# Optimization experiments

Measured on AMD Instinct MI355X. Metric: run time of the kernel, lower is better.

## Reference

```python
import jax, jax.numpy as jnp
import numpy as np
from jax import lax

NAG = 3          # hardcoded in the torch module (query slices, catted_torches)
B = 4096         # batch_size per agent
H = 128          # hidden_dim
HEADS = 8
AD = H // HEADS  # attend_dim
STATE, ACT, SCAN = 48, 2, 256
OUTF, HID = 10, 256
NFEAT = 32 * (SCAN - 6)  # conv output features (two VALID convs: k5 then k3)
EPS = 1e-5

def leaky(x):
    return jnp.where(x >= 0, x, 0.01 * x)

def setup_inputs() -> dict:
    key = jax.random.key(0)
    ks = iter(jax.random.split(key, 40))
    def rn(shape, scale=0.05):
        return jax.random.normal(next(ks), shape, dtype=jnp.float32) * scale
    return {
        'obs':  jax.random.normal(next(ks), (NAG * B, STATE), jnp.float32),
        'acts': jax.random.normal(next(ks), (NAG * B, ACT), jnp.float32),
        'scan': jax.random.normal(next(ks), (NAG * B, SCAN), jnp.float32),
        'conv_w1': rn((32, 1, 5)),  'conv_b1': jnp.zeros((32,), jnp.float32),
        'conv_w2': rn((32, 32, 3)), 'conv_b2': jnp.zeros((32,), jnp.float32),
        'fc_w1': rn((256, NFEAT), 0.01), 'fc_b1': jnp.zeros((256,), jnp.float32),
        'fc_w2': rn((OUTF, 256)),        'fc_b2': jnp.zeros((OUTF,), jnp.float32),
        'enc_w': rn((H, STATE + ACT + OUTF)), 'enc_b': jnp.zeros((H,), jnp.float32),
        'Wk': rn((HEADS, AD, H)),
        'Wv': rn((HEADS, AD, H)), 'bv': jnp.zeros((HEADS, AD), jnp.float32),
        'Wq': rn((NAG, HEADS, AD, H)),
        'q1_w1': rn((HID, 2 * H)), 'q1_b1': jnp.zeros((HID,), jnp.float32),
        'q1_w2': rn((HID, HID)),   'q1_b2': jnp.zeros((HID,), jnp.float32),
        'q1_w3': rn((1, HID)),     'q1_b3': jnp.zeros((1,), jnp.float32),
        'q2_w1': rn((HID, 2 * H)), 'q2_b1': jnp.zeros((HID,), jnp.float32),
        'q2_w2': rn((HID, HID)),   'q2_b2': jnp.zeros((HID,), jnp.float32),
        'q2_w3': rn((1, HID)),     'q2_b3': jnp.zeros((1,), jnp.float32),
    }

def reference(obs, acts, scan, conv_w1, conv_b1, conv_w2, conv_b2,
              fc_w1, fc_b1, fc_w2, fc_b2, enc_w, enc_b, Wk, Wv, bv, Wq,
              q1_w1, q1_b1, q1_w2, q1_b2, q1_w3, q1_b3,
              q2_w1, q2_b1, q2_w2, q2_b2, q2_w3, q2_b3):
    dn = ('NCH', 'OIH', 'NCH')
    x = scan[:, None, :]                                            # [N,1,L]
    x = lax.conv_general_dilated(x, conv_w1, (1,), 'VALID', dimension_numbers=dn)
    x = jax.nn.relu(x + conv_b1[None, :, None])
    x = lax.conv_general_dilated(x, conv_w2, (1,), 'VALID', dimension_numbers=dn)
    x = jax.nn.relu(x + conv_b2[None, :, None])
    x = x.reshape(x.shape[0], -1)                                   # [N, NFEAT]
    x = jax.nn.relu(x @ fc_w1.T + fc_b1)
    feats = x @ fc_w2.T + fc_b2                                     # [N, OUTF]

    inps = jnp.concatenate([obs, acts, feats], axis=1)
    mu, var = inps.mean(0), inps.var(0)                             # BatchNorm1d (train, no affine)
    normed = (inps - mu) / jnp.sqrt(var + EPS)
    sa = leaky(normed @ enc_w.T + enc_b).reshape(NAG, B, H)         # [ag,B,H]

    keys = jnp.einsum('gbh,ndh->ngbd', sa, Wk)                      # [hd,ag,B,ad]
    vals = leaky(jnp.einsum('gbh,ndh->ngbd', sa, Wv) + bv[:, None, None, :])
    q = jnp.einsum('gbh,gndh->gnbd', sa, Wq)                        # [ag,hd,B,ad]

    logits = jnp.einsum('gnbd,nobd->gnbo', q, keys) / np.sqrt(AD)   # [ag,hd,B,ag]
    self_mask = jnp.eye(NAG, dtype=bool)[:, None, None, :]          # exclude own agent
    logits = jnp.where(self_mask, -jnp.inf, logits)
    w = jax.nn.softmax(logits, axis=-1)
    other = jnp.einsum('gnbo,nobd->gnbd', w, vals)                  # [ag,hd,B,ad]
    other = other.transpose(0, 2, 1, 3).reshape(NAG, B, H)          # heads concatenated

    emb = jnp.concatenate([sa, other], axis=2).reshape(NAG * B, 2 * H)

    def mlp(x, w1, b1, w2, b2, w3, b3):
        x = jax.nn.relu(x @ w1.T + b1)
        x = jax.nn.relu(x @ w2.T + b2)
        return x @ w3.T + b3

    q1 = mlp(emb, q1_w1, q1_b1, q1_w2, q1_b2, q1_w3, q1_b3)
    q2 = mlp(emb, q2_w1, q2_b1, q2_w2, q2_b2, q2_w3, q2_b3)
    return (q1, q2)
```

## Files before the change

kernel.cpp:

```cpp
#include <hip/hip_runtime.h>
#include <hip/hip_bf16.h>
#include <cstdint>
#include <cstddef>

typedef unsigned short u16;
typedef __attribute__((ext_vector_type(8))) __bf16 bf16x8;
typedef __attribute__((ext_vector_type(4))) float f32x4;

__device__ __forceinline__ u16 f2b(float f) {
  __hip_bfloat16 h = __float2bfloat16(f);
  return *reinterpret_cast<u16*>(&h);
}
__device__ __forceinline__ uint32_t pk2(float a, float b) {
  __hip_bfloat162 h = __float22bfloat162_rn(make_float2(a, b));
  return *reinterpret_cast<uint32_t*>(&h);
}
__device__ __forceinline__ float b2f(u16 u) {
  union { float f; uint32_t i; } x; x.i = ((uint32_t)u) << 16; return x.f;
}
__device__ __forceinline__ f32x4 mfma16(bf16x8 a, bf16x8 b, f32x4 c) {
  return __builtin_amdgcn_mfma_f32_16x16x32_bf16(a, b, c, 0, 0, 0);
}
__device__ __forceinline__ void async16(const void* g, void* l) {
  __builtin_amdgcn_global_load_lds((const __attribute__((address_space(1))) uint32_t*)g,
                                   (__attribute__((address_space(3))) uint32_t*)l, 16, 0, 0);
}

__global__ __launch_bounds__(256) void w1_perm(const float* __restrict__ w,
                                               u16* __restrict__ o) {
  __shared__ float L[8000];
  int j = blockIdx.x, tid = threadIdx.x;
  for (int i = tid; i < 8000; i += 256) L[i] = w[(size_t)j * 8000 + i];
  __syncthreads();
  for (int i = tid; i < 8000; i += 256) {
    int tt = i >> 5, c2 = i & 31;
    o[(size_t)j * 8000 + i] = f2b(L[c2 * 250 + tt]);
  }
}

struct CvtArgs {
  const float* src[8];
  u16* dst[8];
  int cum[9];
};
__global__ __launch_bounds__(256) void f2b_multi(CvtArgs a, float* stats) {
  int i = blockIdx.x * 256 + threadIdx.x;
  if (blockIdx.x == 0 && threadIdx.x < 128) stats[threadIdx.x] = 0.f;
  int seg = 0;
  #pragma unroll
  for (int s = 1; s < 8; ++s) if (i >= a.cum[s]) seg = s;
  if (i < a.cum[8]) {
    int off = i - a.cum[seg];
    if (seg == 7) {
      int c2 = off / 96, rem = off - c2 * 96, kk = rem >> 5, c1 = rem & 31;
      a.dst[7][off] = f2b(a.src[7][(c2 * 32 + c1) * 3 + kk]);
    } else {
      a.dst[seg][off] = f2b(a.src[seg][off]);
    }
  }
}

__global__ __launch_bounds__(256) void conv_fused(
    const float* __restrict__ scan, const float* __restrict__ cw1,
    const float* __restrict__ cb1, const u16* __restrict__ w2g,
    const float* __restrict__ cb2, u16* __restrict__ x, int row0) {
  __shared__ float s[260];
  __shared__ __align__(16) u16 h1T[258 * 40];
  int tid = threadIdx.x;
  int lrow = blockIdx.x;
  int lane = tid & 63, wv = tid >> 6;
  int l15 = lane & 15, quad = lane >> 4;
  s[tid] = scan[(size_t)(row0 + lrow) * 256 + tid];
  if (tid < 4) s[256 + tid] = 0.f;
  if (tid < 240) h1T[252 * 40 + tid] = 0;
  bf16x8 wfrag[2][3];
  #pragma unroll
  for (int i = 0; i < 2; ++i)
    #pragma unroll
    for (int kk = 0; kk < 3; ++kk)
      wfrag[i][kk] = *(const bf16x8*)&w2g[(i * 16 + l15) * 96 + kk * 32 + quad * 8];
  float bias[2][4];
  #pragma unroll
  for (int i = 0; i < 2; ++i)
    #pragma unroll
    for (int r = 0; r < 4; ++r) bias[i][r] = cb2[i * 16 + quad * 4 + r];
  __syncthreads();
  {
    int cpair = tid & 15, pr = tid >> 4;
    int c0 = cpair * 2;
    float wA[5], wB[5];
    #pragma unroll
    for (int k = 0; k < 5; ++k) { wA[k] = cw1[c0 * 5 + k]; wB[k] = cw1[c0 * 5 + 5 + k]; }
    float bA = cb1[c0], bB = cb1[c0 + 1];
    float sv[20];
    int p0 = pr * 16;
    #pragma unroll
    for (int j = 0; j < 5; ++j) {
      f32x4 v = *(const f32x4*)&s[p0 + 4 * j];
      sv[4 * j] = v[0]; sv[4 * j + 1] = v[1]; sv[4 * j + 2] = v[2]; sv[4 * j + 3] = v[3];
    }
    #pragma unroll
    for (int ii = 0; ii < 16; ++ii) {
      float va = bA, vb = bB;
      #pragma unroll
      for (int k = 0; k < 5; ++k) {
        va += sv[ii + k] * wA[k];
        vb += sv[ii + k] * wB[k];
      }
      int p = p0 + ii;
      if (p < 252) {
        *(uint32_t*)&h1T[p * 40 + c0] = pk2(fmaxf(va, 0.f), fmaxf(vb, 0.f));
      }
    }
  }
  __syncthreads();
  f32x4 zero = {0.f, 0.f, 0.f, 0.f};
  f32x4 acc[4][2];
  #pragma unroll
  for (int jj = 0; jj < 4; ++jj) { acc[jj][0] = zero; acc[jj][1] = zero; }
  #pragma unroll
  for (int kk = 0; kk < 3; ++kk) {
    #pragma unroll
    for (int jj = 0; jj < 4; ++jj) {
      int t = (wv * 4 + jj) * 16 + l15 + kk;
      bf16x8 h = *(const bf16x8*)&h1T[t * 40 + quad * 8];
      acc[jj][0] = mfma16(wfrag[0][kk], h, acc[jj][0]);
      acc[jj][1] = mfma16(wfrag[1][kk], h, acc[jj][1]);
    }
  }
  __syncthreads();
  #pragma unroll
  for (int jj = 0; jj < 4; ++jj) {
    int t = (wv * 4 + jj) * 16 + l15;
    if (t < 250) {
      #pragma unroll
      for (int i = 0; i < 2; ++i) {
        float v0 = fmaxf(acc[jj][i][0] + bias[i][0], 0.f);
        float v1 = fmaxf(acc[jj][i][1] + bias[i][1], 0.f);
        float v2 = fmaxf(acc[jj][i][2] + bias[i][2], 0.f);
        float v3 = fmaxf(acc[jj][i][3] + bias[i][3], 0.f);
        uint2 pr2; pr2.x = pk2(v0, v1); pr2.y = pk2(v2, v3);
        *(uint2*)&h1T[t * 40 + i * 16 + quad * 4] = pr2;
      }
    }
  }
  __syncthreads();
  u16* xr = x + (size_t)lrow * 8000;
  #pragma unroll
  for (int it = 0; it < 4; ++it) {
    int e0 = (it * 256 + tid) * 8;
    if (e0 < 8000) {
      int t = e0 >> 5, c8 = (e0 >> 3) & 3;
      bf16x8 v = *(const bf16x8*)&h1T[t * 40 + c8 * 8];
      *(bf16x8*)&xr[e0] = v;
    }
  }
}

template <int MODE>
__global__ __launch_bounds__(256) void gemm_bt(
    const u16* __restrict__ A, int lda, const u16* __restrict__ W,
    const float* __restrict__ bias, float* __restrict__ outF,
    u16* __restrict__ outB, int ldo, int nst, int wq_sel, size_t out_zoff) {
  __shared__ __align__(16) u16 As[2][128 * 64];
  __shared__ __align__(16) u16 Bs[2][128 * 64];
  int tid = threadIdx.x;
  int m0 = blockIdx.y * 128, n0 = blockIdx.x * 128;
  if (wq_sel) W += (size_t)(blockIdx.y >> 5) * wq_sel;
  int kbase = blockIdx.z * nst * 64;
  if (MODE == 0) outF += (size_t)blockIdx.z * out_zoff;
  const u16* Ap = A + (size_t)m0 * lda + kbase;
  const u16* Wp = W + (size_t)n0 * lda + kbase;
  int lane = tid & 63, wv = tid >> 6;
  int l15 = lane & 15, quad = lane >> 4;
  int wm = (wv >> 1) * 64, wn = (wv & 1) * 64;
  f32x4 zero = {0.f, 0.f, 0.f, 0.f};
  f32x4 acc[4][4];
  #pragma unroll
  for (int i = 0; i < 4; ++i)
    #pragma unroll
    for (int j = 0; j < 4; ++j) acc[i][j] = zero;

  int srow[4], soff[4], sdst[4];
  #pragma unroll
  for (int it = 0; it < 4; ++it) {
    int c = it * 256 + tid;
    int row = c >> 3, slot = c & 7;
    srow[it] = row;
    soff[it] = ((slot ^ (row & 7)) * 8);
    sdst[it] = c * 8;
  }
  int rslot[2];
  rslot[0] = ((quad ^ (l15 & 7)) * 8);
  rslot[1] = (((4 + quad) ^ (l15 & 7)) * 8);

  #pragma unroll 1
  for (int st = 0; st < nst; ++st) {
    if (st == 0) {
      #pragma unroll
      for (int it = 0; it < 4; ++it) {
        async16(Ap + (size_t)srow[it] * lda + soff[it], &As[0][sdst[it]]);
        async16(Wp + (size_t)srow[it] * lda + soff[it], &Bs[0][sdst[it]]);
      }
    }
    __syncthreads();
    if (st + 1 < nst) {
      const u16* An = Ap + (st + 1) * 64;
      const u16* Wn = Wp + (st + 1) * 64;
      u16* Ad = &As[(st + 1) & 1][0];
      u16* Bd = &Bs[(st + 1) & 1][0];
      #pragma unroll
      for (int it = 0; it < 4; ++it) {
        async16(An + (size_t)srow[it] * lda + soff[it], Ad + sdst[it]);
        async16(Wn + (size_t)srow[it] * lda + soff[it], Bd + sdst[it]);
      }
    }
    const u16* Ab = &As[st & 1][0];
    const u16* Bb = &Bs[st & 1][0];
    #pragma unroll
    for (int s = 0; s < 2; ++s) {
      bf16x8 af[4], bfr[4];
      #pragma unroll
      for (int i = 0; i < 4; ++i)
        af[i] = *(const bf16x8*)&Ab[(wm + i * 16 + l15) * 64 + rslot[s]];
      #pragma unroll
      for (int j = 0; j < 4; ++j)
        bfr[j] = *(const bf16x8*)&Bb[(wn + j * 16 + l15) * 64 + rslot[s]];
      #pragma unroll
      for (int i = 0; i < 4; ++i)
        #pragma unroll
        for (int j = 0; j < 4; ++j) acc[i][j] = mfma16(af[i], bfr[j], acc[i][j]);
    }
  }
  #pragma unroll
  for (int i = 0; i < 4; ++i) {
    int mb = m0 + wm + i * 16 + quad * 4;
    #pragma unroll
    for (int j = 0; j < 4; ++j) {
      int n = n0 + wn + j * 16 + l15;
      float bv_ = (MODE == 1 || MODE == 2) ? bias[n] : 0.f;
      #pragma unroll
      for (int r = 0; r < 4; ++r) {
        float v = acc[i][j][r];
        if (MODE == 0) {
          outF[(size_t)(mb + r) * ldo + n] = v;
        } else {
          v += bv_;
          if (MODE == 1) v = fmaxf(v, 0.f);
          if (MODE == 2) v = v >= 0.f ? v : 0.01f * v;
          outB[(size_t)(mb + r) * ldo + n] = f2b(v);
        }
      }
    }
  }
}

__global__ __launch_bounds__(256) void fc2_stats(
    const float* __restrict__ hparts, const float* __restrict__ b1,
    const float* __restrict__ w2, const float* __restrict__ b2,
    const float* __restrict__ obs, const float* __restrict__ acts,
    float* __restrict__ inps, float* __restrict__ stats) {
  __shared__ float hL[32 * 260];
  __shared__ float w2L[10 * 260];
  __shared__ float b1L[256];
  __shared__ float ipL[32 * 61];
  int tid = threadIdx.x, r0 = blockIdx.x * 32;
  b1L[tid] = b1[tid];
  for (int i = tid; i < 2560; i += 256) w2L[(i >> 8) * 260 + (i & 255)] = w2[i];
  for (int i = tid; i < 32 * 48; i += 256) {
    int r = i / 48, f = i - r * 48;
    ipL[r * 61 + f] = obs[(size_t)(r0 + r) * 48 + f];
  }
  if (tid < 64) {
    int r = tid >> 1, f = tid & 1;
    ipL[r * 61 + 48 + f] = acts[(size_t)(r0 + r) * 2 + f];
  }
  __syncthreads();
  const size_t HS = (size_t)12288 * 256;
  for (int i = tid; i < 32 * 256; i += 256) {
    int r = i >> 8, c = i & 255;
    size_t g = (size_t)(r0 + r) * 256 + c;
    float v = b1L[c] + hparts[g] + hparts[g + HS] + hparts[g + 2 * HS] +
              hparts[g + 3 * HS] + hparts[g + 4 * HS];
    hL[r * 260 + c] = fmaxf(v, 0.f);
  }
  __syncthreads();
  {
    int r = tid >> 3, ob = tid & 7;
    for (int o = ob; o < 10; o += 8) {
      float a = 0.f;
      #pragma unroll 8
      for (int c = 0; c < 256; ++c) a += hL[r * 260 + c] * w2L[o * 260 + c];
      ipL[r * 61 + 50 + o] = a + b2[o];
    }
  }
  __syncthreads();
  for (int i = tid; i < 32 * 60; i += 256) {
    int r = i / 60, f = i - r * 60;
    inps[(size_t)(r0 + r) * 64 + f] = ipL[r * 61 + f];
  }
  if (tid < 60) {
    float s = 0.f, s2 = 0.f;
    for (int r = 0; r < 32; ++r) {
      float v = ipL[r * 61 + tid];
      s += v; s2 += v * v;
    }
    atomicAdd(&stats[tid], s);
    atomicAdd(&stats[64 + tid], s2);
  }
}

__global__ __launch_bounds__(256) void enc_kernel(
    const float* __restrict__ inps, const float* __restrict__ stats,
    const float* __restrict__ enc_w, const float* __restrict__ enc_b,
    u16* __restrict__ sab) {
  __shared__ float ewL[128 * 61];
  __shared__ float nrm[32 * 61];
  __shared__ float ebL[128];
  __shared__ float muL[60], ivL[60];
  int tid = threadIdx.x, r0 = blockIdx.x * 32;
  if (tid < 128) ebL[tid] = enc_b[tid];
  if (tid < 60) {
    float s = stats[tid], s2 = stats[64 + tid];
    float mu = s * (1.f / 12288.f);
    float var = s2 * (1.f / 12288.f) - mu * mu;
    muL[tid] = mu;
    ivL[tid] = rsqrtf(var + 1e-5f);
  }
  for (int i = tid; i < 128 * 60; i += 256) {
    int h = i / 60, f = i - h * 60;
    ewL[h * 61 + f] = enc_w[i];
  }
  __syncthreads();
  for (int i = tid; i < 32 * 60; i += 256) {
    int r = i / 60, f = i - r * 60;
    nrm[r * 61 + f] = (inps[(size_t)(r0 + r) * 64 + f] - muL[f]) * ivL[f];
  }
  __syncthreads();
  for (int i = tid; i < 32 * 128; i += 256) {
    int r = i >> 7, h = i & 127;
    float a = ebL[h];
    #pragma unroll 4
    for (int f = 0; f < 60; ++f) a += nrm[r * 61 + f] * ewL[h * 61 + f];
    a = a >= 0.f ? a : 0.01f * a;
    sab[(size_t)(r0 + r) * 128 + h] = f2b(a);
  }
}

__global__ __launch_bounds__(128) void attn_combine(
    const u16* __restrict__ qb, const u16* __restrict__ keysb,
    const u16* __restrict__ valsb, const u16* __restrict__ sab,
    u16* __restrict__ emb) {
  __shared__ float qL[3][128], kL[3][128], vL[3][128];
  __shared__ float lg[3][8][3], wgt[3][8][3];
  int b = blockIdx.x, t = threadIdx.x;
  #pragma unroll
  for (int o = 0; o < 3; ++o) {
    size_t base = (size_t)(o * 4096 + b) * 128 + t;
    qL[o][t] = b2f(qb[base]);
    kL[o][t] = b2f(keysb[base]);
    vL[o][t] = b2f(valsb[base]);
  }
  __syncthreads();
  if (t < 72) {
    int g = t / 24, n = (t / 3) % 8, o = t % 3;
    float a = 0.f;
    #pragma unroll
    for (int d = 0; d < 16; ++d) a += qL[g][n * 16 + d] * kL[o][n * 16 + d];
    lg[g][n][o] = (o == g) ? -1e30f : a * 0.25f;
  }
  __syncthreads();
  if (t < 24) {
    int g = t / 8, n = t % 8;
    float m = fmaxf(fmaxf(lg[g][n][0], lg[g][n][1]), lg[g][n][2]);
    float e0 = expf(lg[g][n][0] - m), e1 = expf(lg[g][n][1] - m),
          e2 = expf(lg[g][n][2] - m);
    float inv = 1.f / (e0 + e1 + e2);
    wgt[g][n][0] = e0 * inv; wgt[g][n][1] = e1 * inv; wgt[g][n][2] = e2 * inv;
  }
  __syncthreads();
  int n = t >> 4, d = t & 15;
  #pragma unroll
  for (int g = 0; g < 3; ++g) {
    float o_ = wgt[g][n][0] * vL[0][n * 16 + d] +
               wgt[g][n][1] * vL[1][n * 16 + d] +
               wgt[g][n][2] * vL[2][n * 16 + d];
    size_t rbase = (size_t)(g * 4096 + b) * 256;
    emb[rbase + 128 + t] = f2b(o_);
    emb[rbase + t] = sab[(size_t)(g * 4096 + b) * 128 + t];
  }
}

__global__ __launch_bounds__(256) void final_dot(
    const u16* __restrict__ t2a, const u16* __restrict__ t2b,
    const float* __restrict__ w3a, const float* __restrict__ b3a,
    const float* __restrict__ w3b, const float* __restrict__ b3b,
    float* __restrict__ out) {
  int wv = threadIdx.x >> 6, lane = threadIdx.x & 63;
  int row = blockIdx.x * 4 + wv;
  float sa_ = 0.f, sb_ = 0.f;
  #pragma unroll
  for (int e = 0; e < 4; ++e) {
    int c = lane * 4 + e;
    sa_ += b2f(t2a[(size_t)row * 256 + c]) * w3a[c];
    sb_ += b2f(t2b[(size_t)row * 256 + c]) * w3b[c];
  }
  #pragma unroll
  for (int off = 32; off; off >>= 1) {
    sa_ += __shfl_down(sa_, off);
    sb_ += __shfl_down(sb_, off);
  }
  if (lane == 0) {
    out[row] = sa_ + b3a[0];
    out[12288 + row] = sb_ + b3b[0];
  }
}

extern "C" void kernel_launch(void* const* d_in, const int* in_sizes, int n_in,
                              void* d_out, int out_size, void* d_ws,
                              size_t ws_size, hipStream_t stream) {
  const float* obs  = (const float*)d_in[0];
  const float* acts = (const float*)d_in[1];
  const float* scan = (const float*)d_in[2];
  const float* cw1  = (const float*)d_in[3];
  const float* cb1  = (const float*)d_in[4];
  const float* cw2  = (const float*)d_in[5];
  const float* cb2  = (const float*)d_in[6];
  const float* fw1  = (const float*)d_in[7];
  const float* fb1  = (const float*)d_in[8];
  const float* fw2  = (const float*)d_in[9];
  const float* fb2  = (const float*)d_in[10];
  const float* encw = (const float*)d_in[11];
  const float* encb = (const float*)d_in[12];
  const float* Wk   = (const float*)d_in[13];
  const float* Wv   = (const float*)d_in[14];
  const float* bv   = (const float*)d_in[15];
  const float* Wq   = (const float*)d_in[16];
  const float* q1w1 = (const float*)d_in[17];
  const float* q1b1 = (const float*)d_in[18];
  const float* q1w2 = (const float*)d_in[19];
  const float* q1b2 = (const float*)d_in[20];
  const float* q1w3 = (const float*)d_in[21];
  const float* q1b3 = (const float*)d_in[22];
  const float* q2w1 = (const float*)d_in[23];
  const float* q2b1 = (const float*)d_in[24];
  const float* q2w2 = (const float*)d_in[25];
  const float* q2b2 = (const float*)d_in[26];
  const float* q2w3 = (const float*)d_in[27];
  const float* q2b3 = (const float*)d_in[28];
  float* out = (float*)d_out;
  char* ws = (char*)d_ws;
  if (ws_size < 166009856u) return;

  u16*   x     = (u16*)(ws + 0);
  u16*   w1b   = (u16*)(ws + 98304000);
  float* hpart = (float*)(ws + 102400000);
  float* stats = (float*)(ws + 165314560);
  u16*   wkb   = (u16*)(ws + 165315584);
  u16*   wvb   = (u16*)(ws + 165348352);
  u16*   wqb   = (u16*)(ws + 165381120);
  u16*   m1a   = (u16*)(ws + 165479424);
  u16*   m2a   = (u16*)(ws + 165610496);
  u16*   m1b   = (u16*)(ws + 165741568);
  u16*   m2b   = (u16*)(ws + 165872640);
  u16*   w2g   = (u16*)(ws + 166003712);
  float* inps  = (float*)(ws + 0);
  u16*   sab   = (u16*)(ws + 3145728);
  u16*   keysb = (u16*)(ws + 6291456);
  u16*   valsb = (u16*)(ws + 9437184);
  u16*   qb    = (u16*)(ws + 12582912);
  u16*   embb  = (u16*)(ws + 15728640);
  u16*   t1a   = (u16*)(ws + 22020096);
  u16*   t2a   = (u16*)(ws + 28311552);
  u16*   t1b   = (u16*)(ws + 34603008);
  u16*   t2b   = (u16*)(ws + 40894464);

  w1_perm<<<256, 256, 0, stream>>>(fw1, w1b);
  CvtArgs ca;
  ca.src[0] = Wk;  ca.src[1] = Wv;  ca.src[2] = Wq;  ca.src[3] = q1w1;
  ca.src[4] = q1w2; ca.src[5] = q2w1; ca.src[6] = q2w2; ca.src[7] = cw2;
  ca.dst[0] = wkb; ca.dst[1] = wvb; ca.dst[2] = wqb; ca.dst[3] = m1a;
  ca.dst[4] = m2a; ca.dst[5] = m1b; ca.dst[6] = m2b; ca.dst[7] = w2g;
  const int sz[8] = {16384, 16384, 49152, 65536, 65536, 65536, 65536, 3072};
  int cum = 0;
  ca.cum[0] = 0;
  for (int i = 0; i < 8; ++i) { cum += sz[i]; ca.cum[i + 1] = cum; }
  f2b_multi<<<(cum + 255) / 256, 256, 0, stream>>>(ca, stats);

  for (int s = 0; s < 2; ++s) {
    conv_fused<<<6144, 256, 0, stream>>>(scan, cw1, cb1, w2g, cb2, x, s * 6144);
    gemm_bt<0><<<dim3(2, 48, 5), 256, 0, stream>>>(
        x, 8000, w1b, nullptr, hpart + (size_t)s * 6144 * 256, nullptr, 256,
        25, 0, (size_t)12288 * 256);
  }
  fc2_stats<<<384, 256, 0, stream>>>(hpart, fb1, fw2, fb2, obs, acts, inps, stats);
  enc_kernel<<<384, 256, 0, stream>>>(inps, stats, encw, encb, sab);
  gemm_bt<3><<<dim3(1, 96, 1), 256, 0, stream>>>(sab, 128, wkb, nullptr, nullptr,
                                                 keysb, 128, 2, 0, 0);
  gemm_bt<2><<<dim3(1, 96, 1), 256, 0, stream>>>(sab, 128, wvb, bv, nullptr,
                                                 valsb, 128, 2, 0, 0);
  gemm_bt<3><<<dim3(1, 96, 1), 256, 0, stream>>>(sab, 128, wqb, nullptr, nullptr,
                                                 qb, 128, 2, 16384, 0);
  attn_combine<<<4096, 128, 0, stream>>>(qb, keysb, valsb, sab, embb);
  gemm_bt<1><<<dim3(2, 96, 1), 256, 0, stream>>>(embb, 256, m1a, q1b1, nullptr,
                                                 t1a, 256, 4, 0, 0);
  gemm_bt<1><<<dim3(2, 96, 1), 256, 0, stream>>>(t1a, 256, m2a, q1b2, nullptr,
                                                 t2a, 256, 4, 0, 0);
  gemm_bt<1><<<dim3(2, 96, 1), 256, 0, stream>>>(embb, 256, m1b, q2b1, nullptr,
                                                 t1b, 256, 4, 0, 0);
  gemm_bt<1><<<dim3(2, 96, 1), 256, 0, stream>>>(t1b, 256, m2b, q2b2, nullptr,
                                                 t2b, 256, 4, 0, 0);
  final_dot<<<3072, 256, 0, stream>>>(t2a, t2b, q1w3, q1b3, q2w3, q2b3, out);
}
```

Before: 379.9 us.

## Run conv1 on MFMA, write conv output directly, and batch twin Q-MLP GEMMs

The first convolution (k=5, single input channel) moves from scalar FMAs to a bf16 MFMA, using a zero-padded im2col tile in LDS and a pre-converted padded weight matrix. The second conv's epilogue writes bf16 results straight to global memory, removing an LDS staging pass and a barrier. The two Q-network MLPs are merged into two wider GEMM launches over concatenated weights, using a per-block A-offset for the second layer, which cuts the number of launches. The price is extra LDS for the im2col tile, rounding conv1 inputs to bf16, and uncoalesced 8-byte global stores in the conv epilogue.

```diff
diff --git a/kernel.cpp b/kernel.cpp
--- a/kernel.cpp
+++ b/kernel.cpp
@@ -39,138 +39,152 @@
 }
 
 struct CvtArgs {
-  const float* src[8];
-  u16* dst[8];
-  int cum[9];
+  const float* src[13];
+  void* dst[13];
+  int cum[14];
+  int kind[13];
 };
 __global__ __launch_bounds__(256) void f2b_multi(CvtArgs a, float* stats) {
   int i = blockIdx.x * 256 + threadIdx.x;
   if (blockIdx.x == 0 && threadIdx.x < 128) stats[threadIdx.x] = 0.f;
   int seg = 0;
   #pragma unroll
-  for (int s = 1; s < 8; ++s) if (i >= a.cum[s]) seg = s;
-  if (i < a.cum[8]) {
+  for (int s = 1; s < 13; ++s) if (i >= a.cum[s]) seg = s;
+  if (i < a.cum[13]) {
     int off = i - a.cum[seg];
-    if (seg == 7) {
+    int kind = a.kind[seg];
+    const float* src = a.src[seg];
+    if (kind == 0) {
+      ((u16*)a.dst[seg])[off] = f2b(src[off]);
+    } else if (kind == 1) {
       int c2 = off / 96, rem = off - c2 * 96, kk = rem >> 5, c1 = rem & 31;
-      a.dst[7][off] = f2b(a.src[7][(c2 * 32 + c1) * 3 + kk]);
+      ((u16*)a.dst[seg])[off] = f2b(src[(c2 * 32 + c1) * 3 + kk]);
+    } else if (kind == 2) {
+      int c1 = off >> 5, k = off & 31;
+      ((u16*)a.dst[seg])[off] = f2b(k < 5 ? src[c1 * 5 + k] : 0.f);
     } else {
-      a.dst[seg][off] = f2b(a.src[seg][off]);
+      ((float*)a.dst[seg])[off] = src[off];
     }
   }
 }
 
 __global__ __launch_bounds__(256) void conv_fused(
-    const float* __restrict__ scan, const float* __restrict__ cw1,
+    const float* __restrict__ scan, const u16* __restrict__ w1g,
     const float* __restrict__ cb1, const u16* __restrict__ w2g,
     const float* __restrict__ cb2, u16* __restrict__ x, int row0) {
   __shared__ float s[260];
+  __shared__ __align__(16) u16 A1[256 * 40];
   __shared__ __align__(16) u16 h1T[258 * 40];
   int tid = threadIdx.x;
-  int lrow = blockIdx.x;
   int lane = tid & 63, wv = tid >> 6;
   int l15 = lane & 15, quad = lane >> 4;
-  s[tid] = scan[(size_t)(row0 + lrow) * 256 + tid];
+  s[tid] = scan[(size_t)(row0 + blockIdx.x) * 256 + tid];
   if (tid < 4) s[256 + tid] = 0.f;
-  if (tid < 240) h1T[252 * 40 + tid] = 0;
-  bf16x8 wfrag[2][3];
+  if (tid < 80) h1T[256 * 40 + tid] = 0;
+  bf16x8 w1f[2];
+  w1f[0] = *(const bf16x8*)&w1g[l15 * 32 + quad * 8];
+  w1f[1] = *(const bf16x8*)&w1g[(16 + l15) * 32 + quad * 8];
+  bf16x8 w2f[2][3];
   #pragma unroll
   for (int i = 0; i < 2; ++i)
     #pragma unroll
     for (int kk = 0; kk < 3; ++kk)
-      wfrag[i][kk] = *(const bf16x8*)&w2g[(i * 16 + l15) * 96 + kk * 32 + quad * 8];
-  float bias[2][4];
+      w2f[i][kk] = *(const bf16x8*)&w2g[(i * 16 + l15) * 96 + kk * 32 + quad * 8];
+  float cb1v[2][4], cb2v[2][4];
   #pragma unroll
   for (int i = 0; i < 2; ++i)
     #pragma unroll
-    for (int r = 0; r < 4; ++r) bias[i][r] = cb2[i * 16 + quad * 4 + r];
+    for (int r = 0; r < 4; ++r) {
+      cb1v[i][r] = cb1[i * 16 + quad * 4 + r];
+      cb2v[i][r] = cb2[i * 16 + quad * 4 + r];
+    }
   __syncthreads();
   {
-    int cpair = tid & 15, pr = tid >> 4;
-    int c0 = cpair * 2;
-    float wA[5], wB[5];
-    #pragma unroll
-    for (int k = 0; k < 5; ++k) { wA[k] = cw1[c0 * 5 + k]; wB[k] = cw1[c0 * 5 + 5 + k]; }
-    float bA = cb1[c0], bB = cb1[c0 + 1];
-    float sv[20];
-    int p0 = pr * 16;
-    #pragma unroll
-    for (int j = 0; j < 5; ++j) {
-      f32x4 v = *(const f32x4*)&s[p0 + 4 * j];
-      sv[4 * j] = v[0]; sv[4 * j + 1] = v[1]; sv[4 * j + 2] = v[2]; sv[4 * j + 3] = v[3];
-    }
-    #pragma unroll
-    for (int ii = 0; ii < 16; ++ii) {
-      float va = bA, vb = bB;
-      #pragma unroll
-      for (int k = 0; k < 5; ++k) {
-        va += sv[ii + k] * wA[k];
-        vb += sv[ii + k] * wB[k];
+    union { bf16x8 v; u16 u[8]; } pk;
+    #pragma unroll
+    for (int k = 0; k < 5; ++k) pk.u[k] = f2b(s[tid + k]);
+    pk.u[5] = 0; pk.u[6] = 0; pk.u[7] = 0;
+    *(bf16x8*)&A1[tid * 40] = pk.v;
+    uint4 z = make_uint4(0, 0, 0, 0);
+    *(uint4*)&A1[tid * 40 + 8] = z;
+    *(uint4*)&A1[tid * 40 + 16] = z;
+    *(uint4*)&A1[tid * 40 + 24] = z;
+  }
+  __syncthreads();
+  f32x4 zero = {0.f, 0.f, 0.f, 0.f};
+  {
+    f32x4 acc1[4][2];
+    #pragma unroll
+    for (int nt = 0; nt < 4; ++nt) { acc1[nt][0] = zero; acc1[nt][1] = zero; }
+    #pragma unroll
+    for (int nt = 0; nt < 4; ++nt) {
+      int p = (wv * 4 + nt) * 16 + l15;
+      bf16x8 bfr = *(const bf16x8*)&A1[p * 40 + quad * 8];
+      acc1[nt][0] = mfma16(w1f[0], bfr, acc1[nt][0]);
+      acc1[nt][1] = mfma16(w1f[1], bfr, acc1[nt][1]);
+    }
+    #pragma unroll
+    for (int nt = 0; nt < 4; ++nt) {
+      int p = (wv * 4 + nt) * 16 + l15;
+      #pragma unroll
+      for (int mt = 0; mt < 2; ++mt) {
+        float v0 = fmaxf(acc1[nt][mt][0] + cb1v[mt][0], 0.f);
+        float v1 = fmaxf(acc1[nt][mt][1] + cb1v[mt][1], 0.f);
+        float v2 = fmaxf(acc1[nt][mt][2] + cb1v[mt][2], 0.f);
+        float v3 = fmaxf(acc1[nt][mt][3] + cb1v[mt][3], 0.f);
+        uint2 u; u.x = pk2(v0, v1); u.y = pk2(v2, v3);
+        *(uint2*)&h1T[p * 40 + mt * 16 + quad * 4] = u;
       }
-      int p = p0 + ii;
-      if (p < 252) {
-        *(uint32_t*)&h1T[p * 40 + c0] = pk2(fmaxf(va, 0.f), fmaxf(vb, 0.f));
-      }
-    }
-  }
-  __syncthreads();
-  f32x4 zero = {0.f, 0.f, 0.f, 0.f};
-  f32x4 acc[4][2];
-  #pragma unroll
-  for (int jj = 0; jj < 4; ++jj) { acc[jj][0] = zero; acc[jj][1] = zero; }
+    }
+  }
+  __syncthreads();
+  f32x4 acc2[4][2];
+  #pragma unroll
+  for (int jj = 0; jj < 4; ++jj) { acc2[jj][0] = zero; acc2[jj][1] = zero; }
   #pragma unroll
   for (int kk = 0; kk < 3; ++kk) {
     #pragma unroll
     for (int jj = 0; jj < 4; ++jj) {
       int t = (wv * 4 + jj) * 16 + l15 + kk;
       bf16x8 h = *(const bf16x8*)&h1T[t * 40 + quad * 8];
-      acc[jj][0] = mfma16(wfrag[0][kk], h, acc[jj][0]);
-      acc[jj][1] = mfma16(wfrag[1][kk], h, acc[jj][1]);
-    }
-  }
-  __syncthreads();
+      acc2[jj][0] = mfma16(w2f[0][kk], h, acc2[jj][0]);
+      acc2[jj][1] = mfma16(w2f[1][kk], h, acc2[jj][1]);
+    }
+  }
+  u16* xr = x + (size_t)blockIdx.x * 8000;
   #pragma unroll
   for (int jj = 0; jj < 4; ++jj) {
     int t = (wv * 4 + jj) * 16 + l15;
     if (t < 250) {
       #pragma unroll
       for (int i = 0; i < 2; ++i) {
-        float v0 = fmaxf(acc[jj][i][0] + bias[i][0], 0.f);
-        float v1 = fmaxf(acc[jj][i][1] + bias[i][1], 0.f);
-        float v2 = fmaxf(acc[jj][i][2] + bias[i][2], 0.f);
-        float v3 = fmaxf(acc[jj][i][3] + bias[i][3], 0.f);
-        uint2 pr2; pr2.x = pk2(v0, v1); pr2.y = pk2(v2, v3);
-        *(uint2*)&h1T[t * 40 + i * 16 + quad * 4] = pr2;
+        float v0 = fmaxf(acc2[jj][i][0] + cb2v[i][0], 0.f);
+        float v1 = fmaxf(acc2[jj][i][1] + cb2v[i][1], 0.f);
+        float v2 = fmaxf(acc2[jj][i][2] + cb2v[i][2], 0.f);
+        float v3 = fmaxf(acc2[jj][i][3] + cb2v[i][3], 0.f);
+        uint2 u; u.x = pk2(v0, v1); u.y = pk2(v2, v3);
+        *(uint2*)&xr[t * 32 + i * 16 + quad * 4] = u;
       }
-    }
-  }
-  __syncthreads();
-  u16* xr = x + (size_t)lrow * 8000;
-  #pragma unroll
-  for (int it = 0; it < 4; ++it) {
-    int e0 = (it * 256 + tid) * 8;
-    if (e0 < 8000) {
-      int t = e0 >> 5, c8 = (e0 >> 3) & 3;
-      bf16x8 v = *(const bf16x8*)&h1T[t * 40 + c8 * 8];
-      *(bf16x8*)&xr[e0] = v;
     }
   }
 }
 
 template <int MODE>
 __global__ __launch_bounds__(256) void gemm_bt(
-    const u16* __restrict__ A, int lda, const u16* __restrict__ W,
+    const u16* __restrict__ A, int lda, const u16* __restrict__ W, int ldw,
     const float* __restrict__ bias, float* __restrict__ outF,
-    u16* __restrict__ outB, int ldo, int nst, int wq_sel, size_t out_zoff) {
+    u16* __restrict__ outB, int ldo, int nst, int wq_sel, int a_sel,
+    size_t out_zoff) {
   __shared__ __align__(16) u16 As[2][128 * 64];
   __shared__ __align__(16) u16 Bs[2][128 * 64];
   int tid = threadIdx.x;
   int m0 = blockIdx.y * 128, n0 = blockIdx.x * 128;
   if (wq_sel) W += (size_t)(blockIdx.y >> 5) * wq_sel;
+  if (a_sel) A += (size_t)(blockIdx.x >> 1) * a_sel;
   int kbase = blockIdx.z * nst * 64;
   if (MODE == 0) outF += (size_t)blockIdx.z * out_zoff;
   const u16* Ap = A + (size_t)m0 * lda + kbase;
-  const u16* Wp = W + (size_t)n0 * lda + kbase;
+  const u16* Wp = W + (size_t)n0 * ldw + kbase;
   int lane = tid & 63, wv = tid >> 6;
   int l15 = lane & 15, quad = lane >> 4;
   int wm = (wv >> 1) * 64, wn = (wv & 1) * 64;
@@ -200,7 +214,7 @@
       #pragma unroll
       for (int it = 0; it < 4; ++it) {
         async16(Ap + (size_t)srow[it] * lda + soff[it], &As[0][sdst[it]]);
-        async16(Wp + (size_t)srow[it] * lda + soff[it], &Bs[0][sdst[it]]);
+        async16(Wp + (size_t)srow[it] * ldw + soff[it], &Bs[0][sdst[it]]);
       }
     }
     __syncthreads();
@@ -212,7 +226,7 @@
       #pragma unroll
       for (int it = 0; it < 4; ++it) {
         async16(An + (size_t)srow[it] * lda + soff[it], Ad + sdst[it]);
-        async16(Wn + (size_t)srow[it] * lda + soff[it], Bd + sdst[it]);
+        async16(Wn + (size_t)srow[it] * ldw + soff[it], Bd + sdst[it]);
       }
     }
     const u16* Ab = &As[st & 1][0];
@@ -392,18 +406,17 @@
 }
 
 __global__ __launch_bounds__(256) void final_dot(
-    const u16* __restrict__ t2a, const u16* __restrict__ t2b,
-    const float* __restrict__ w3a, const float* __restrict__ b3a,
-    const float* __restrict__ w3b, const float* __restrict__ b3b,
-    float* __restrict__ out) {
+    const u16* __restrict__ t2ab, const float* __restrict__ w3a,
+    const float* __restrict__ b3a, const float* __restrict__ w3b,
+    const float* __restrict__ b3b, float* __restrict__ out) {
   int wv = threadIdx.x >> 6, lane = threadIdx.x & 63;
   int row = blockIdx.x * 4 + wv;
   float sa_ = 0.f, sb_ = 0.f;
   #pragma unroll
   for (int e = 0; e < 4; ++e) {
     int c = lane * 4 + e;
-    sa_ += b2f(t2a[(size_t)row * 256 + c]) * w3a[c];
-    sb_ += b2f(t2b[(size_t)row * 256 + c]) * w3b[c];
+    sa_ += b2f(t2ab[(size_t)row * 512 + c]) * w3a[c];
+    sb_ += b2f(t2ab[(size_t)row * 512 + 256 + c]) * w3b[c];
   }
   #pragma unroll
   for (int off = 32; off; off >>= 1) {
@@ -450,7 +463,7 @@
   const float* q2b3 = (const float*)d_in[28];
   float* out = (float*)d_out;
   char* ws = (char*)d_ws;
-  if (ws_size < 166009856u) return;
+  if (ws_size < 166016000u) return;
 
   u16*   x     = (u16*)(ws + 0);
   u16*   w1b   = (u16*)(ws + 98304000);
@@ -459,56 +472,56 @@
   u16*   wkb   = (u16*)(ws + 165315584);
   u16*   wvb   = (u16*)(ws + 165348352);
   u16*   wqb   = (u16*)(ws + 165381120);
-  u16*   m1a   = (u16*)(ws + 165479424);
-  u16*   m2a   = (u16*)(ws + 165610496);
-  u16*   m1b   = (u16*)(ws + 165741568);
-  u16*   m2b   = (u16*)(ws + 165872640);
+  u16*   m1ab  = (u16*)(ws + 165479424);
+  u16*   m2ab  = (u16*)(ws + 165741568);
   u16*   w2g   = (u16*)(ws + 166003712);
+  u16*   w1g   = (u16*)(ws + 166009856);
+  float* bc1   = (float*)(ws + 166011904);
+  float* bc2   = (float*)(ws + 166013952);
   float* inps  = (float*)(ws + 0);
   u16*   sab   = (u16*)(ws + 3145728);
   u16*   keysb = (u16*)(ws + 6291456);
   u16*   valsb = (u16*)(ws + 9437184);
   u16*   qb    = (u16*)(ws + 12582912);
   u16*   embb  = (u16*)(ws + 15728640);
-  u16*   t1a   = (u16*)(ws + 22020096);
-  u16*   t2a   = (u16*)(ws + 28311552);
-  u16*   t1b   = (u16*)(ws + 34603008);
-  u16*   t2b   = (u16*)(ws + 40894464);
+  u16*   t1ab  = (u16*)(ws + 22020096);
+  u16*   t2ab  = (u16*)(ws + 34603008);
 
   w1_perm<<<256, 256, 0, stream>>>(fw1, w1b);
   CvtArgs ca;
-  ca.src[0] = Wk;  ca.src[1] = Wv;  ca.src[2] = Wq;  ca.src[3] = q1w1;
-  ca.src[4] = q1w2; ca.src[5] = q2w1; ca.src[6] = q2w2; ca.src[7] = cw2;
-  ca.dst[0] = wkb; ca.dst[1] = wvb; ca.dst[2] = wqb; ca.dst[3] = m1a;
-  ca.dst[4] = m2a; ca.dst[5] = m1b; ca.dst[6] = m2b; ca.dst[7] = w2g;
-  const int sz[8] = {16384, 16384, 49152, 65536, 65536, 65536, 65536, 3072};
+  const float* srcs[13] = {Wk, Wv, Wq, q1w1, q2w1, q1w2, q2w2, cw2, cw1,
+                           q1b1, q2b1, q1b2, q2b2};
+  void* dsts[13] = {wkb, wvb, wqb, m1ab, m1ab + 65536, m2ab, m2ab + 65536,
+                    w2g, w1g, bc1, bc1 + 256, bc2, bc2 + 256};
+  const int sz[13] = {16384, 16384, 49152, 65536, 65536, 65536, 65536,
+                      3072, 1024, 256, 256, 256, 256};
+  const int kinds[13] = {0, 0, 0, 0, 0, 0, 0, 1, 2, 3, 3, 3, 3};
   int cum = 0;
   ca.cum[0] = 0;
-  for (int i = 0; i < 8; ++i) { cum += sz[i]; ca.cum[i + 1] = cum; }
+  for (int i = 0; i < 13; ++i) {
+    ca.src[i] = srcs[i]; ca.dst[i] = dsts[i]; ca.kind[i] = kinds[i];
+    cum += sz[i]; ca.cum[i + 1] = cum;
+  }
   f2b_multi<<<(cum + 255) / 256, 256, 0, stream>>>(ca, stats);
 
   for (int s = 0; s < 2; ++s) {
-    conv_fused<<<6144, 256, 0, stream>>>(scan, cw1, cb1, w2g, cb2, x, s * 6144);
+    conv_fused<<<6144, 256, 0, stream>>>(scan, w1g, cb1, w2g, cb2, x, s * 6144);
     gemm_bt<0><<<dim3(2, 48, 5), 256, 0, stream>>>(
-        x, 8000, w1b, nullptr, hpart + (size_t)s * 6144 * 256, nullptr, 256,
-        25, 0, (size_t)12288 * 256);
+        x, 8000, w1b, 8000, nullptr, hpart + (size_t)s * 6144 * 256, nullptr,
+        256, 25, 0, 0, (size_t)12288 * 256);
   }
   fc2_stats<<<384, 256, 0, stream>>>(hpart, fb1, fw2, fb2, obs, acts, inps, stats);
   enc_kernel<<<384, 256, 0, stream>>>(inps, stats, encw, encb, sab);
-  gemm_bt<3><<<dim3(1, 96, 1), 256, 0, stream>>>(sab, 128, wkb, nullptr, nullptr,
-                                                 keysb, 128, 2, 0, 0);
-  gemm_bt<2><<<dim3(1, 96, 1), 256, 0, stream>>>(sab, 128, wvb, bv, nullptr,
-                                                 valsb, 128, 2, 0, 0);
-  gemm_bt<3><<<dim3(1, 96, 1), 256, 0, stream>>>(sab, 128, wqb, nullptr, nullptr,
-                                                 qb, 128, 2, 16384, 0);
+  gemm_bt<3><<<dim3(1, 96, 1), 256, 0, stream>>>(sab, 128, wkb, 128, nullptr,
+                                                 nullptr, keysb, 128, 2, 0, 0, 0);
+  gemm_bt<2><<<dim3(1, 96, 1), 256, 0, stream>>>(sab, 128, wvb, 128, bv, nullptr,
+                                                 valsb, 128, 2, 0, 0, 0);
+  gemm_bt<3><<<dim3(1, 96, 1), 256, 0, stream>>>(sab, 128, wqb, 128, nullptr,
+                                                 nullptr, qb, 128, 2, 16384, 0, 0);
   attn_combine<<<4096, 128, 0, stream>>>(qb, keysb, valsb, sab, embb);
-  gemm_bt<1><<<dim3(2, 96, 1), 256, 0, stream>>>(embb, 256, m1a, q1b1, nullptr,
-                                                 t1a, 256, 4, 0, 0);
-  gemm_bt<1><<<dim3(2, 96, 1), 256, 0, stream>>>(t1a, 256, m2a, q1b2, nullptr,
-                                                 t2a, 256, 4, 0, 0);
-  gemm_bt<1><<<dim3(2, 96, 1), 256, 0, stream>>>(embb, 256, m1b, q2b1, nullptr,
-                                                 t1b, 256, 4, 0, 0);
-  gemm_bt<1><<<dim3(2, 96, 1), 256, 0, stream>>>(t1b, 256, m2b, q2b2, nullptr,
-                                                 t2b, 256, 4, 0, 0);
-  final_dot<<<3072, 256, 0, stream>>>(t2a, t2b, q1w3, q1b3, q2w3, q2b3, out);
-}
+  gemm_bt<1><<<dim3(4, 96, 1), 256, 0, stream>>>(embb, 256, m1ab, 256, bc1,
+                                                 nullptr, t1ab, 512, 4, 0, 0, 0);
+  gemm_bt<1><<<dim3(4, 96, 1), 256, 0, stream>>>(t1ab, 512, m2ab, 256, bc2,
+                                                 nullptr, t2ab, 512, 4, 0, 256, 0);
+  final_dot<<<3072, 256, 0, stream>>>(t2ab, q1w3, q1b3, q2w3, q2b3, out);
+}
```

Measured after the change: 358.2 us. -5.7%, faster.
